# Kernel optimization log

Hardware: AMD Instinct MI355X
Metric: run time of the kernel (lower is better)

## Reference

```python
import jax, jax.numpy as jnp
import numpy as np

B, S, H = 2, 2048, 2048
E, K, HID = 8, 2, 4096          # num_experts, top-k, expert hidden (2*H)
NH, HD = 8, 256                  # attention heads, head_dim
MS, MD = 256, 512                # memory_size, memory_dim
RSTEPS, RD = 3, 512              # reasoning steps, reasoning_dim
SCALE = 16.0                     # sqrt(head_dim)


def setup_inputs() -> dict:
    key = jax.random.key(0)
    ks = iter(jax.random.split(key, 64))
    def w(shape, s=0.02):
        return (jax.random.normal(next(ks), shape, jnp.float32) * s)
    z = lambda *shape: jnp.zeros(shape, jnp.float32)
    inp = {
        'hidden_states': jax.random.normal(next(ks), (B, S, H), jnp.float32),
        'attention_mask': jnp.zeros((B, S), jnp.float32),  # 0 = unmasked (faithful: mask*-1e9 added)
        # MoE
        'gate_w': w((H, E)), 'gate_b': z(E),
        'moe_w1': w((E, H, HID)), 'moe_b1': z(E, HID),
        'moe_w2': w((E, HID, H)), 'moe_b2': z(E, H),
        # memory-augmented attention
        'q_w': w((H, H)), 'q_b': z(H),
        'k_w': w((H, H)), 'k_b': z(H),
        'v_w': w((H, H)), 'v_b': z(H),
        'o_w': w((H, H)), 'o_b': z(H),
        'mem_values': jax.random.normal(next(ks), (MS, MD), jnp.float32),
        'mem_proj_w': w((MD, H)), 'mem_proj_b': z(H),
        'mem_attn_w': w((H, MS)), 'mem_attn_b': z(MS),
        # hierarchical reasoning (stacked over steps)
        'rs_w1': w((RSTEPS, H, RD)), 'rs_b1': z(RSTEPS, RD),
        'rs_w2': w((RSTEPS, RD, H)), 'rs_b2': z(RSTEPS, H),
        'ln_g': jnp.ones((RSTEPS, H), jnp.float32), 'ln_b': z(RSTEPS, H),
        'hg_w1': w((RSTEPS, H, H // 4)), 'hg_b1': z(RSTEPS, H // 4),
        'hg_w2': w((RSTEPS, H // 4, 1)), 'hg_b2': z(RSTEPS, 1),
        'integ_w': w((RSTEPS * H, H)), 'integ_b': z(H),
    }
    return inp


def _layernorm(x, g, b, eps=1e-5):
    m = x.mean(-1, keepdims=True)
    v = ((x - m) ** 2).mean(-1, keepdims=True)
    return (x - m) / jnp.sqrt(v + eps) * g + b


def _forward(hidden_states, attention_mask, gate_w, gate_b, moe_w1, moe_b1, moe_w2, moe_b2,
             q_w, q_b, k_w, k_b, v_w, v_b, o_w, o_b, mem_values, mem_proj_w, mem_proj_b,
             mem_attn_w, mem_attn_b, rs_w1, rs_b1, rs_w2, rs_b2, ln_g, ln_b,
             hg_w1, hg_b1, hg_w2, hg_b2, integ_w, integ_b):
    h = hidden_states
    N = B * S
    # ---- Mixture of Experts (top-k routing, dense combine-weight formulation) ----
    x_flat = h.reshape(N, H)
    gate_probs = jax.nn.softmax(x_flat @ gate_w + gate_b, axis=-1)        # [N,E]
    topk_s, topk_i = jax.lax.top_k(gate_probs, K)                          # [N,K]
    topk_p = jax.nn.softmax(topk_s, axis=-1)                               # renormalize over top-k
    comb = jnp.zeros((N, E), x_flat.dtype).at[jnp.arange(N)[:, None], topk_i].add(topk_p)
    h1 = jax.nn.relu(jnp.einsum('nd,edh->neh', x_flat, moe_w1) + moe_b1)   # [N,E,HID]
    eo = jnp.einsum('neh,ehd->ned', h1, moe_w2) + moe_b2                   # [N,E,H]
    moe_out = jnp.einsum('ned,ne->nd', eo, comb).reshape(B, S, H)
    h = h + 0.5 * moe_out
    # ---- Memory-augmented attention ----
    q = (h @ q_w + q_b).reshape(B, S, NH, HD).transpose(0, 2, 1, 3)
    k = (h @ k_w + k_b).reshape(B, S, NH, HD).transpose(0, 2, 1, 3)
    v = (h @ v_w + v_b).reshape(B, S, NH, HD).transpose(0, 2, 1, 3)
    scores = jnp.einsum('bhqd,bhkd->bhqk', q, k) / SCALE
    scores = scores + attention_mask[:, None, None, :] * (-1e9)
    probs = jax.nn.softmax(scores, axis=-1)
    attn = jnp.einsum('bhqk,bhkd->bhqd', probs, v).transpose(0, 2, 1, 3).reshape(B, S, H)
    mem_p = jax.nn.softmax(h @ mem_attn_w + mem_attn_b, axis=-1)           # [B,S,MS]
    mem_o = (mem_p @ mem_values) @ mem_proj_w + mem_proj_b                 # [B,S,H]
    mem_out = (attn + 0.3 * mem_o) @ o_w + o_b
    h = h + mem_out
    # ---- Hierarchical reasoning ----
    cur = h
    outs = []
    for i in range(RSTEPS):
        so = jax.nn.relu(cur @ rs_w1[i] + rs_b1[i]) @ rs_w2[i] + rs_b2[i]
        so = _layernorm(so, ln_g[i], ln_b[i])
        g = jax.nn.sigmoid(jax.nn.relu(cur @ hg_w1[i] + hg_b1[i]) @ hg_w2[i] + hg_b2[i])  # [B,S,1]
        cur = cur + g * so
        outs.append(cur)
    final = jnp.concatenate(outs, axis=-1) @ integ_w + integ_b
    return h + final


def reference(hidden_states, attention_mask, gate_w, gate_b, moe_w1, moe_b1, moe_w2, moe_b2,
              q_w, q_b, k_w, k_b, v_w, v_b, o_w, o_b, mem_values, mem_proj_w, mem_proj_b,
              mem_attn_w, mem_attn_b, rs_w1, rs_b1, rs_w2, rs_b2, ln_g, ln_b,
              hg_w1, hg_b1, hg_w2, hg_b2, integ_w, integ_b):
    return _forward(hidden_states, attention_mask, gate_w, gate_b, moe_w1, moe_b1, moe_w2, moe_b2,
                    q_w, q_b, k_w, k_b, v_w, v_b, o_w, o_b, mem_values, mem_proj_w, mem_proj_b,
                    mem_attn_w, mem_attn_b, rs_w1, rs_b1, rs_w2, rs_b2, ln_g, ln_b,
                    hg_w1, hg_b1, hg_w2, hg_b2, integ_w, integ_b)
```

## Files before the change

### kernel.cpp

```cpp
#include <hip/hip_runtime.h>
#include <string.h>


typedef __attribute__((ext_vector_type(4))) float f32x4;
typedef __attribute__((ext_vector_type(8))) __bf16 bf16x8;

#define NTOK 4096
#define HDIM 2048
#define AS1 __attribute__((address_space(1)))
#define AS3 __attribute__((address_space(3)))

__device__ __forceinline__ unsigned short f2bf(float f) {
  unsigned u = __float_as_uint(f);
  unsigned r = (u + 0x7fffu + ((u >> 16) & 1u)) >> 16;
  return (unsigned short)r;
}
__device__ __forceinline__ float bf2f(unsigned short u) {
  return __uint_as_float(((unsigned)u) << 16);
}
__device__ __forceinline__ void unpack8(uint4 r, float* v) {
  v[0]=bf2f((unsigned short)(r.x&0xffff)); v[1]=bf2f((unsigned short)(r.x>>16));
  v[2]=bf2f((unsigned short)(r.y&0xffff)); v[3]=bf2f((unsigned short)(r.y>>16));
  v[4]=bf2f((unsigned short)(r.z&0xffff)); v[5]=bf2f((unsigned short)(r.z>>16));
  v[6]=bf2f((unsigned short)(r.w&0xffff)); v[7]=bf2f((unsigned short)(r.w>>16));
}
__device__ __forceinline__ uint4 pack8(const float* v) {
  uint4 r;
  r.x = (unsigned)f2bf(v[0]) | ((unsigned)f2bf(v[1])<<16);
  r.y = (unsigned)f2bf(v[2]) | ((unsigned)f2bf(v[3])<<16);
  r.z = (unsigned)f2bf(v[4]) | ((unsigned)f2bf(v[5])<<16);
  r.w = (unsigned)f2bf(v[6]) | ((unsigned)f2bf(v[7])<<16);
  return r;
}

__global__ void k_tconv(const float* __restrict__ in, unsigned short* __restrict__ out,
                        int R, int C, long inB, long outB) {
  __shared__ float tl[32][33];
  const int z = blockIdx.z;
  const float* ip = in + (long)z * inB;
  unsigned short* op = out + (long)z * outB;
  const int tx = threadIdx.x & 31, ty = threadIdx.x >> 5;
  const int c0 = blockIdx.x * 32, r0 = blockIdx.y * 32;
#pragma unroll
  for (int i = 0; i < 4; i++)
    tl[ty + i*8][tx] = ip[(long)(r0 + ty + i*8) * C + c0 + tx];
  __syncthreads();
#pragma unroll
  for (int i = 0; i < 4; i++)
    op[(long)(c0 + ty + i*8) * R + r0 + tx] = f2bf(tl[tx][ty + i*8]);
}

__global__ void k_tconv4(const float* __restrict__ i0, const float* __restrict__ i1,
                         const float* __restrict__ i2, const float* __restrict__ i3,
                         unsigned short* __restrict__ out) {
  __shared__ float tl[32][33];
  const int z = blockIdx.z;
  const float* ip = (z == 0) ? i0 : (z == 1) ? i1 : (z == 2) ? i2 : i3;
  unsigned short* op = out + (size_t)z * 2048 * 2048;
  const int tx = threadIdx.x & 31, ty = threadIdx.x >> 5;
  const int c0 = blockIdx.x * 32, r0 = blockIdx.y * 32;
#pragma unroll
  for (int i = 0; i < 4; i++)
    tl[ty + i*8][tx] = ip[(long)(r0 + ty + i*8) * 2048 + c0 + tx];
  __syncthreads();
#pragma unroll
  for (int i = 0; i < 4; i++)
    op[(long)(c0 + ty + i*8) * 2048 + r0 + tx] = f2bf(tl[tx][ty + i*8]);
}

__global__ void k_cvt(const float* __restrict__ in, unsigned short* __restrict__ out, long n4) {
  long i = (long)blockIdx.x * blockDim.x + threadIdx.x;
  if (i < n4) {
    float4 v = ((const float4*)in)[i];
    float vv[4] = {v.x, v.y, v.z, v.w};
    union { unsigned short u[4]; uint2 d; } p;
#pragma unroll
    for (int j = 0; j < 4; j++) p.u[j] = f2bf(vv[j]);
    ((uint2*)out)[i] = p.d;
  }
}

__global__ void k_tvact(const unsigned short* __restrict__ qkv, unsigned short* __restrict__ vT) {
  __shared__ unsigned short tl[32][33];
  const int z = blockIdx.z, b = z >> 3, hh = z & 7;
  const unsigned short* ip = qkv + (long)b * 2048 * 6144 + 4096 + hh * 256;
  unsigned short* op = vT + (long)z * 256 * 2048;
  const int tx = threadIdx.x & 31, ty = threadIdx.x >> 5;
  const int d0 = blockIdx.x * 32, s0 = blockIdx.y * 32;
#pragma unroll
  for (int i = 0; i < 4; i++)
    tl[ty + i*8][tx] = ip[(long)(s0 + ty + i*8) * 6144 + d0 + tx];
  __syncthreads();
#pragma unroll
  for (int i = 0; i < 4; i++)
    op[(long)(d0 + ty + i*8) * 2048 + s0 + tx] = tl[tx][ty + i*8];
}

__global__ void k_misc(const float* __restrict__ mask, float* __restrict__ mv,
                       const float* __restrict__ qb, const float* __restrict__ kb,
                       const float* __restrict__ vb, float* __restrict__ qkvb,
                       const float* __restrict__ rsb1, const float* __restrict__ hgb1,
                       float* __restrict__ rhb, int* __restrict__ meta) {
  const int b = blockIdx.x, t = threadIdx.x;
  if (b < 16) {
    int i = b * 256 + t; mv[i] = -1e9f * mask[i];
  } else if (b < 40) {
    int i = (b - 16) * 256 + t;
    qkvb[i] = (i < 2048) ? qb[i] : (i < 4096) ? kb[i - 2048] : vb[i - 4096];
  } else if (b < 46) {
    int i = (b - 40) * 256 + t;
    int s = i >> 9, c = i & 511;
    rhb[s * 1024 + c] = rsb1[i]; rhb[s * 1024 + 512 + c] = hgb1[i];
  } else {
    if (t < 8) meta[t] = 0;
  }
}

__global__ void k_gate(const float* __restrict__ x, const float* __restrict__ gw,
                       const float* __restrict__ gb, int* __restrict__ meta,
                       int* __restrict__ e0a, int* __restrict__ e1a,
                       float* __restrict__ w0a, float* __restrict__ w1a) {
  const int wv = threadIdx.x >> 6, ln = threadIdx.x & 63;
  const int n = blockIdx.x * 4 + wv;
  const float* xr = x + (long)n * HDIM;
  float s[8] = {0,0,0,0,0,0,0,0};
  for (int k = ln; k < HDIM; k += 64) {
    float xv = xr[k];
    const float* g = gw + (long)k * 8;
#pragma unroll
    for (int e = 0; e < 8; e++) s[e] += xv * g[e];
  }
#pragma unroll
  for (int e = 0; e < 8; e++)
    for (int d = 32; d; d >>= 1) s[e] += __shfl_xor(s[e], d);
  if (ln == 0) {
    float mx = -1e30f;
#pragma unroll
    for (int e = 0; e < 8; e++) { s[e] += gb[e]; mx = fmaxf(mx, s[e]); }
    float p[8], sum = 0.f;
#pragma unroll
    for (int e = 0; e < 8; e++) { p[e] = expf(s[e] - mx); sum += p[e]; }
    float inv = 1.f / sum;
#pragma unroll
    for (int e = 0; e < 8; e++) p[e] *= inv;
    int e0 = 0;
    for (int e = 1; e < 8; e++) if (p[e] > p[e0]) e0 = e;
    int e1 = (e0 == 0) ? 1 : 0;
    for (int e = 0; e < 8; e++) if (e != e0 && p[e] > p[e1]) e1 = e;
    float q = expf(p[e1] - p[e0]);
    float w0 = 1.f / (1.f + q), w1 = q / (1.f + q);
    e0a[n] = e0; e1a[n] = e1; w0a[n] = w0; w1a[n] = w1;
    atomicAdd(&meta[e0], 1); atomicAdd(&meta[e1], 1);
  }
}

__global__ void k_buildmap(int* meta) {
  if (threadIdx.x == 0 && blockIdx.x == 0) {
    int cum = 0, nT = 0;
    for (int e = 0; e < 8; e++) {
      int c = meta[e];
      meta[16 + e] = cum; meta[24 + e] = cum + c; meta[8 + e] = 0;
      int t = (c + 127) >> 7;
      for (int i = 0; i < t; i++) { meta[33 + nT] = e; meta[129 + nT] = cum + i * 128; nT++; }
      cum += c;
    }
    meta[32] = nT;
  }
}

__global__ void k_scatter(int* __restrict__ meta, const int* __restrict__ e0a,
                          const int* __restrict__ e1a, int* __restrict__ s0a,
                          int* __restrict__ s1a, int* __restrict__ srcTok) {
  const int n = blockIdx.x * 256 + threadIdx.x;
  if (n < NTOK) {
    int e0 = e0a[n], e1 = e1a[n];
    int s0 = meta[16 + e0] + atomicAdd(&meta[8 + e0], 1);
    int s1 = meta[16 + e1] + atomicAdd(&meta[8 + e1], 1);
    s0a[n] = s0; s1a[n] = s1; srcTok[s0] = n; srcTok[s1] = n;
  }
}

__global__ void k_combine(const float* __restrict__ h, const unsigned short* __restrict__ eo,
                          const int* __restrict__ s0a, const int* __restrict__ s1a,
                          const float* __restrict__ w0a, const float* __restrict__ w1a,
                          unsigned short* __restrict__ h2b) {
  const int n = blockIdx.x, c = threadIdx.x * 8;
  const float w0 = w0a[n], w1 = w1a[n];
  uint4 a = *(const uint4*)(eo + (long)s0a[n] * HDIM + c);
  uint4 b = *(const uint4*)(eo + (long)s1a[n] * HDIM + c);
  float va[8], vb[8]; unpack8(a, va); unpack8(b, vb);
  const float* hr = h + (long)n * HDIM + c;
  float o[8];
#pragma unroll
  for (int j = 0; j < 8; j++) o[j] = hr[j] + 0.5f * (w0 * va[j] + w1 * vb[j]);
  *(uint4*)(h2b + (long)n * HDIM + c) = pack8(o);
}

__global__ void k_softmax256(const float* __restrict__ in, unsigned short* __restrict__ out) {
  const int wv = threadIdx.x >> 6, ln = threadIdx.x & 63;
  const long r = (long)blockIdx.x * 4 + wv;
  const float4 v4 = ((const float4*)(in + r * 256))[ln];
  float v[4] = {v4.x, v4.y, v4.z, v4.w};
  float m = fmaxf(fmaxf(v[0], v[1]), fmaxf(v[2], v[3]));
  for (int d = 32; d; d >>= 1) m = fmaxf(m, __shfl_xor(m, d));
  float s = 0.f;
#pragma unroll
  for (int j = 0; j < 4; j++) { v[j] = expf(v[j] - m); s += v[j]; }
  for (int d = 32; d; d >>= 1) s += __shfl_xor(s, d);
  const float inv = 1.f / s;
  union { unsigned short u[4]; uint2 d2; } p;
#pragma unroll
  for (int j = 0; j < 4; j++) p.u[j] = f2bf(v[j] * inv);
  ((uint2*)(out + r * 256))[ln] = p.d2;
}

__global__ void k_gdot(const unsigned short* __restrict__ g1, long ld, const float* __restrict__ w,
                       const float* __restrict__ bb, float* __restrict__ gv) {
  const int wv = threadIdx.x >> 6, ln = threadIdx.x & 63;
  const int n = blockIdx.x * 4 + wv;
  uint4 raw = *(const uint4*)(g1 + (long)n * ld + ln * 8);
  float v[8]; unpack8(raw, v);
  const float4 wa = ((const float4*)w)[ln * 2];
  const float4 wb = ((const float4*)w)[ln * 2 + 1];
  float s = v[0]*wa.x + v[1]*wa.y + v[2]*wa.z + v[3]*wa.w
          + v[4]*wb.x + v[5]*wb.y + v[6]*wb.z + v[7]*wb.w;
  for (int d = 32; d; d >>= 1) s += __shfl_xor(s, d);
  if (ln == 0) gv[n] = 1.f / (1.f + expf(-(s + bb[0])));
}

__global__ void k_lnupdate(const float* __restrict__ so, const float* __restrict__ curIn,
                           const float* __restrict__ gv, const float* __restrict__ lng,
                           const float* __restrict__ lnb, float* __restrict__ curOut,
                           unsigned short* __restrict__ curbOut, unsigned short* __restrict__ outs,
                           int step) {
  const int n = blockIdx.x, t = threadIdx.x, wv = t >> 6, ln = t & 63, c = t * 8;
  const float* row = so + (long)n * 2048 + c;
  float x[8];
#pragma unroll
  for (int j = 0; j < 8; j++) x[j] = row[j];
  float s1 = 0.f, s2 = 0.f;
#pragma unroll
  for (int j = 0; j < 8; j++) { s1 += x[j]; s2 += x[j] * x[j]; }
  for (int d = 32; d; d >>= 1) { s1 += __shfl_xor(s1, d); s2 += __shfl_xor(s2, d); }
  __shared__ float a1[4], a2[4];
  if (ln == 0) { a1[wv] = s1; a2[wv] = s2; }
  __syncthreads();
  s1 = a1[0] + a1[1] + a1[2] + a1[3];
  s2 = a2[0] + a2[1] + a2[2] + a2[3];
  const float mean = s1 * (1.f / 2048.f);
  const float var = s2 * (1.f / 2048.f) - mean * mean;
  const float rstd = rsqrtf(var + 1e-5f);
  const float g = gv[n];
  const float* ci = curIn + (long)n * 2048 + c;
  float o[8];
#pragma unroll
  for (int j = 0; j < 8; j++) {
    float l = (x[j] - mean) * rstd * lng[c + j] + lnb[c + j];
    o[j] = ci[j] + g * l;
  }
  float* co = curOut + (long)n * 2048 + c;
#pragma unroll
  for (int j = 0; j < 8; j++) co[j] = o[j];
  *(uint4*)(curbOut + (long)n * 2048 + c) = pack8(o);
  *(uint4*)(outs + (long)n * 6144 + (long)step * 2048 + c) = pack8(o);
}

struct GArgs {
  const unsigned short* A; long lda, aSO, aSI;
  const unsigned short* Bt; long ldb, bSO, bSI;
  int M, N, K;
  const float* adv; long advSO, advSI;
  float alpha, rscale;
  const float* rF; long ldrF, rfSO, rfSI;
  const unsigned short* rB; long ldrB, rbSO, rbSI;
  float* oF; long ldoF, ofSO, ofSI;
  unsigned short* oB; long ldoB, obSO, obSI;
  const int* meta;
  const int* srcTok;
};

template <int MOE, int RELU, int RESID, int OUTF, int OUTB>
__global__ __launch_bounds__(512) void gemm_bt(GArgs g) {
  __shared__ unsigned short lds[2 * 16384];
  const int t = threadIdx.x, wv = t >> 6, ln = t & 63, ln15 = ln & 15;
  const int lr8 = ln >> 3;
  const int lsl = (ln & 7) ^ lr8;
  const int bz = blockIdx.z;
  int row0, rowMax;
  const unsigned short *A, *Bt;
  long advO = 0, rFO = 0, rBO = 0, oFO = 0, oBO = 0;
  if constexpr (MOE) {
    const int ty = blockIdx.y;
    if (ty >= g.meta[32]) return;
    const int e = g.meta[33 + ty];
    row0 = g.meta[129 + ty]; rowMax = g.meta[24 + e];
    A = g.A; Bt = g.Bt + (long)e * g.bSO;
    advO = (long)e * g.advSO;
  } else {
    row0 = blockIdx.y << 7; rowMax = g.M;
    const long bo = (long)(bz >> 3), bi = (long)(bz & 7);
    A = g.A + bo * g.aSO + bi * g.aSI;
    Bt = g.Bt + bo * g.bSO + bi * g.bSI;
    advO = bo * g.advSO + bi * g.advSI;
    rFO = bo * g.rfSO + bi * g.rfSI;
    rBO = bo * g.rbSO + bi * g.rbSI;
    oFO = bo * g.ofSO + bi * g.ofSI;
    oBO = bo * g.obSO + bi * g.obSI;
  }
  const int col0 = blockIdx.x << 7;
  const long lda = g.lda, ldb = g.ldb;
  const int wm = (wv >> 2) << 6;
  const int wc = (wv & 3) << 5;

  int grow0, grow1;
  {
    int r0i = row0 + (wv << 4) + lr8;
    int r1i = r0i + 8;
    if constexpr (MOE) {
      r0i = (r0i < rowMax) ? r0i : (rowMax - 1);
      r1i = (r1i < rowMax) ? r1i : (rowMax - 1);
    }
    if constexpr (MOE == 2) { grow0 = g.srcTok[r0i]; grow1 = g.srcTok[r1i]; }
    else { grow0 = r0i; grow1 = r1i; }
  }

  auto STAGE = [&](int kt, unsigned base) {
    const long kk = ((long)kt << 6) + (lsl << 3);
    {
      const int rb = (wv << 4);
      __builtin_amdgcn_global_load_lds(
          (const AS1 void*)(A + (long)grow0 * lda + kk),
          (AS3 void*)(lds + base + (rb << 6)), 16, 0, 0);
      __builtin_amdgcn_global_load_lds(
          (const AS1 void*)(A + (long)grow1 * lda + kk),
          (AS3 void*)(lds + base + ((rb + 8) << 6)), 16, 0, 0);
    }
#pragma unroll
    for (int l = 0; l < 2; ++l) {
      const int rb = (wv << 4) + (l << 3);
      __builtin_amdgcn_global_load_lds(
          (const AS1 void*)(Bt + (long)(col0 + rb + lr8) * ldb + kk),
          (AS3 void*)(lds + base + 8192 + (rb << 6)), 16, 0, 0);
    }
  };

  const f32x4 fz = {0.f, 0.f, 0.f, 0.f};
  f32x4 acc[4][2];
#pragma unroll
  for (int i = 0; i < 4; i++)
#pragma unroll
    for (int j = 0; j < 2; j++) acc[i][j] = fz;

  const int nt = g.K >> 6;

  STAGE(0, 0);
  asm volatile("s_waitcnt vmcnt(0)" ::: "memory");
  __builtin_amdgcn_s_barrier();

  for (int kt = 0; kt < nt; ++kt) {
    const unsigned aB = (kt & 1) ? 16384u : 0u;
    const unsigned nB = aB ^ 16384u;
    if (kt + 1 < nt) STAGE(kt + 1, nB);
#pragma unroll
    for (int ks = 0; ks < 2; ++ks) {
      const int kb = (ks << 2) + (ln >> 4);
      bf16x8 bg[2];
#pragma unroll
      for (int j = 0; j < 2; ++j) {
        const int r = wc + (j << 4) + ln15;
        bg[j] = *(const bf16x8*)(lds + aB + 8192 + (r << 6) + ((kb ^ (r & 7)) << 3));
      }
      __builtin_amdgcn_s_setprio(1);
#pragma unroll
      for (int i = 0; i < 4; ++i) {
        const int r = wm + (i << 4) + ln15;
        bf16x8 a = *(const bf16x8*)(lds + aB + (r << 6) + ((kb ^ (r & 7)) << 3));
#pragma unroll
        for (int j = 0; j < 2; ++j)
          acc[i][j] = __builtin_amdgcn_mfma_f32_16x16x32_bf16(a, bg[j], acc[i][j], 0, 0, 0);
      }
      __builtin_amdgcn_s_setprio(0);
    }
    asm volatile("s_waitcnt vmcnt(0)" ::: "memory");
    __builtin_amdgcn_s_barrier();
  }

#pragma unroll
  for (int i = 0; i < 4; i++) {
#pragma unroll
    for (int j = 0; j < 2; j++) {
      const int cc = col0 + wc + (j << 4) + ln15;
      const float av = g.adv ? g.adv[advO + cc] : 0.f;
#pragma unroll
      for (int r = 0; r < 4; r++) {
        const int rr = row0 + wm + (i << 4) + ((ln >> 4) << 2) + r;
        if (rr < rowMax) {
          float v = g.alpha * acc[i][j][r] + av;
          if constexpr (RELU) v = fmaxf(v, 0.f);
          if constexpr (RESID == 1) v = g.rF[rFO + (long)rr * g.ldrF + cc] + g.rscale * v;
          if constexpr (RESID == 2) v = bf2f(g.rB[rBO + (long)rr * g.ldrB + cc]) + g.rscale * v;
          if constexpr (OUTF) g.oF[oFO + (long)rr * g.ldoF + cc] = v;
          if constexpr (OUTB) g.oB[oBO + (long)rr * g.ldoB + cc] = f2bf(v);
        }
      }
    }
  }
}

__global__ __launch_bounds__(512) void k_pv(const unsigned short* __restrict__ S,
                                            const unsigned short* __restrict__ Vt,
                                            unsigned short* __restrict__ O) {
  __shared__ unsigned short lds[4096 + 16384];
  __shared__ float pm[64][8], ps[64][8];
  __shared__ float smax[64], sinv[64];
  const int t = threadIdx.x, wv = t >> 6, ln = t & 63, ln15 = ln & 15;
  const int lr8 = ln >> 3, lk = ln & 7;
  const int lsl = lk ^ lr8;
  const int rt = blockIdx.x, bh = blockIdx.y;
  const int b = bh >> 3, hh = bh & 7;
  const int row0 = rt << 6;
  const unsigned short* Sb = S + (long)bh * 2048 * 2048;
  const unsigned short* Vb = Vt + (long)bh * 256 * 2048;

  {
    const int r = t >> 3, sg = t & 7;
    const unsigned short* p = Sb + (long)(row0 + r) * 2048 + sg * 256;
    float m = -3.0e38f, s = 0.f;
    for (int i = 0; i < 32; ++i) {
      uint4 raw = ((const uint4*)p)[i];
      float v[8]; unpack8(raw, v);
      float m8 = v[0];
#pragma unroll
      for (int j = 1; j < 8; j++) m8 = fmaxf(m8, v[j]);
      const float mn = fmaxf(m, m8);
      s *= expf(m - mn);
#pragma unroll
      for (int j = 0; j < 8; j++) s += expf(v[j] - mn);
      m = mn;
    }
    pm[r][sg] = m; ps[r][sg] = s;
  }
  __syncthreads();
  if (t < 64) {
    float m = pm[t][0];
#pragma unroll
    for (int j = 1; j < 8; j++) m = fmaxf(m, pm[t][j]);
    float s = 0.f;
#pragma unroll
    for (int j = 0; j < 8; j++) s += ps[t][j] * expf(pm[t][j] - m);
    smax[t] = m; sinv[t] = 1.f / s;
  }
  __syncthreads();
  const int arow = (wv << 3) + lr8;
  const float am = smax[arow], ainv = sinv[arow];

  const f32x4 fz = {0.f, 0.f, 0.f, 0.f};
  f32x4 acc[4][2];
#pragma unroll
  for (int i = 0; i < 4; i++)
#pragma unroll
    for (int j = 0; j < 2; j++) acc[i][j] = fz;

  const int wc = wv << 5;

  for (int kt = 0; kt < 32; ++kt) {
    const long kk = ((long)kt << 6) + (lsl << 3);
    const uint4 araw = *(const uint4*)(Sb + (long)(row0 + arow) * 2048 + kk);
#pragma unroll
    for (int l = 0; l < 4; ++l) {
      const int rb = (l << 6) + (wv << 3);
      __builtin_amdgcn_global_load_lds(
          (const AS1 void*)(Vb + (long)(rb + lr8) * 2048 + kk),
          (AS3 void*)(lds + 4096 + (rb << 6)), 16, 0, 0);
    }
    {
      float v[8]; unpack8(araw, v);
      float pvv[8];
#pragma unroll
      for (int j = 0; j < 8; j++) pvv[j] = expf(v[j] - am) * ainv;
      *(uint4*)(lds + (arow << 6) + (lk << 3)) = pack8(pvv);
    }
    __syncthreads();
#pragma unroll
    for (int ks = 0; ks < 2; ++ks) {
      const int kb = (ks << 2) + (ln >> 4);
      bf16x8 bg[2];
#pragma unroll
      for (int j = 0; j < 2; ++j) {
        const int r = wc + (j << 4) + ln15;
        bg[j] = *(const bf16x8*)(lds + 4096 + (r << 6) + ((kb ^ (r & 7)) << 3));
      }
      __builtin_amdgcn_s_setprio(1);
#pragma unroll
      for (int i = 0; i < 4; ++i) {
        const int r = (i << 4) + ln15;
        bf16x8 a = *(const bf16x8*)(lds + (r << 6) + ((kb ^ (r & 7)) << 3));
#pragma unroll
        for (int j = 0; j < 2; ++j)
          acc[i][j] = __builtin_amdgcn_mfma_f32_16x16x32_bf16(a, bg[j], acc[i][j], 0, 0, 0);
      }
      __builtin_amdgcn_s_setprio(0);
    }
    __syncthreads();
  }

  unsigned short* Ob = O + (long)b * 2048 * 2048 + hh * 256;
#pragma unroll
  for (int i = 0; i < 4; ++i) {
#pragma unroll
    for (int j = 0; j < 2; ++j) {
      const int cc = wc + (j << 4) + ln15;
#pragma unroll
      for (int r = 0; r < 4; ++r) {
        const int rr = row0 + (i << 4) + ((ln >> 4) << 2) + r;
        Ob[(long)rr * 2048 + cc] = f2bf(acc[i][j][r]);
      }
    }
  }
}

static constexpr size_t O_W1T = 0;
static constexpr size_t O_W2T = O_W1T + (size_t)8 * 4096 * 2048 * 2;
static constexpr size_t O_QT  = O_W2T + (size_t)8 * 4096 * 2048 * 2;
static constexpr size_t O_KT  = O_QT + (size_t)2048 * 2048 * 2;
static constexpr size_t O_VWT = O_KT + (size_t)2048 * 2048 * 2;
static constexpr size_t O_OT  = O_VWT + (size_t)2048 * 2048 * 2;
static constexpr size_t O_MAT = O_OT + (size_t)2048 * 2048 * 2;
static constexpr size_t O_MPT = O_MAT + (size_t)256 * 2048 * 2;
static constexpr size_t O_MVT = O_MPT + (size_t)2048 * 512 * 2;
static constexpr size_t O_RH1 = O_MVT + (size_t)512 * 256 * 2;
static constexpr size_t O_RS2 = O_RH1 + (size_t)3 * 1024 * 2048 * 2;
static constexpr size_t O_IGT = O_RS2 + (size_t)3 * 2048 * 512 * 2;
static constexpr size_t O_META= O_IGT + (size_t)2048 * 6144 * 2;
static constexpr size_t O_E0  = O_META + 4096;
static constexpr size_t O_E1  = O_E0 + 16384;
static constexpr size_t O_W0  = O_E1 + 16384;
static constexpr size_t O_W1  = O_W0 + 16384;
static constexpr size_t O_S0  = O_W1 + 16384;
static constexpr size_t O_S1  = O_S0 + 16384;
static constexpr size_t O_SRC = O_S1 + 16384;
static constexpr size_t O_MSK = O_SRC + 32768;
static constexpr size_t O_GV  = O_MSK + 16384;
static constexpr size_t O_QKVB= O_GV + 16384;
static constexpr size_t O_RHB = O_QKVB + 6144 * 4;
static constexpr size_t O_H2  = O_RHB + 3072 * 4;
static constexpr size_t O_H2B = O_H2 + (size_t)4096 * 2048 * 4;
static constexpr size_t O_H3  = O_H2B + (size_t)4096 * 2048 * 2;
static constexpr size_t O_H3B = O_H3 + (size_t)4096 * 2048 * 4;
static constexpr size_t O_ATT = O_H3B + (size_t)4096 * 2048 * 2;
static constexpr size_t O_AO2 = O_ATT + (size_t)4096 * 2048 * 2;
static constexpr size_t O_MLG = O_AO2 + (size_t)4096 * 2048 * 2;
static constexpr size_t O_MPB = O_MLG + (size_t)4096 * 256 * 4;
static constexpr size_t O_MPV = O_MPB + (size_t)4096 * 256 * 2;
static constexpr size_t O_AR  = O_MPV + (size_t)4096 * 512 * 2;
static constexpr size_t O_XB = O_AR;
static constexpr size_t O_XG = O_XB + (size_t)4096 * 2048 * 2;
static constexpr size_t O_H1 = O_XG + (size_t)8192 * 2048 * 2;
static constexpr size_t O_EO = O_H1 + (size_t)8192 * 4096 * 2;
static constexpr size_t O_QB = O_AR;
static constexpr size_t O_VT = O_QB + (size_t)3 * 4096 * 2048 * 2;
static constexpr size_t O_SC = O_VT + (size_t)4096 * 2048 * 2;
static constexpr size_t O_T1 = O_AR;
static constexpr size_t O_SOB= O_T1 + (size_t)4096 * 1024 * 2;
static constexpr size_t O_CUR= O_SOB + (size_t)4096 * 2048 * 4;
static constexpr size_t O_CRB= O_CUR + (size_t)4096 * 2048 * 4;
static constexpr size_t O_OUS= O_CRB + (size_t)4096 * 2048 * 2;

extern "C" void kernel_launch(void* const* d_in, const int* in_sizes, int n_in,
                              void* d_out, int out_size, void* d_ws, size_t ws_size,
                              hipStream_t stream) {
  (void)in_sizes; (void)n_in; (void)out_size; (void)ws_size;
  const float* h        = (const float*)d_in[0];
  const float* mask     = (const float*)d_in[1];
  const float* gate_w   = (const float*)d_in[2];
  const float* gate_b   = (const float*)d_in[3];
  const float* moe_w1   = (const float*)d_in[4];
  const float* moe_b1   = (const float*)d_in[5];
  const float* moe_w2   = (const float*)d_in[6];
  const float* moe_b2   = (const float*)d_in[7];
  const float* q_w      = (const float*)d_in[8];
  const float* q_b      = (const float*)d_in[9];
  const float* k_w      = (const float*)d_in[10];
  const float* k_b      = (const float*)d_in[11];
  const float* v_w      = (const float*)d_in[12];
  const float* v_b      = (const float*)d_in[13];
  const float* o_w      = (const float*)d_in[14];
  const float* o_b      = (const float*)d_in[15];
  const float* mem_vals = (const float*)d_in[16];
  const float* mproj_w  = (const float*)d_in[17];
  const float* mproj_b  = (const float*)d_in[18];
  const float* mattn_w  = (const float*)d_in[19];
  const float* mattn_b  = (const float*)d_in[20];
  const float* rs_w1    = (const float*)d_in[21];
  const float* rs_b1    = (const float*)d_in[22];
  const float* rs_w2    = (const float*)d_in[23];
  const float* rs_b2    = (const float*)d_in[24];
  const float* ln_g     = (const float*)d_in[25];
  const float* ln_b     = (const float*)d_in[26];
  const float* hg_w1    = (const float*)d_in[27];
  const float* hg_b1    = (const float*)d_in[28];
  const float* hg_w2    = (const float*)d_in[29];
  const float* hg_b2    = (const float*)d_in[30];
  const float* integ_w  = (const float*)d_in[31];
  const float* integ_b  = (const float*)d_in[32];

  char* ws = (char*)d_ws;
  auto U = [&](size_t o) { return (unsigned short*)(ws + o); };
  auto F = [&](size_t o) { return (float*)(ws + o); };
  auto I = [&](size_t o) { return (int*)(ws + o); };

  k_tconv<<<dim3(128, 64, 8), 256, 0, stream>>>(moe_w1, U(O_W1T), 2048, 4096, 8388608, 8388608);
  k_tconv<<<dim3(64, 128, 8), 256, 0, stream>>>(moe_w2, U(O_W2T), 4096, 2048, 8388608, 8388608);
  k_tconv4<<<dim3(64, 64, 4), 256, 0, stream>>>(q_w, k_w, v_w, o_w, U(O_QT));
  k_tconv<<<dim3(8, 64, 1), 256, 0, stream>>>(mattn_w, U(O_MAT), 2048, 256, 0, 0);
  k_tconv<<<dim3(64, 16, 1), 256, 0, stream>>>(mproj_w, U(O_MPT), 512, 2048, 0, 0);
  k_tconv<<<dim3(16, 8, 1), 256, 0, stream>>>(mem_vals, U(O_MVT), 256, 512, 0, 0);
  k_tconv<<<dim3(16, 64, 3), 256, 0, stream>>>(rs_w1, U(O_RH1), 2048, 512, 2048 * 512, 1024 * 2048);
  k_tconv<<<dim3(16, 64, 3), 256, 0, stream>>>(hg_w1, U(O_RH1) + (size_t)512 * 2048, 2048, 512,
                                               2048 * 512, 1024 * 2048);
  k_tconv<<<dim3(64, 16, 3), 256, 0, stream>>>(rs_w2, U(O_RS2), 512, 2048, 512 * 2048, 512 * 2048);
  k_tconv<<<dim3(64, 192, 1), 256, 0, stream>>>(integ_w, U(O_IGT), 6144, 2048, 0, 0);
  k_cvt<<<8192, 256, 0, stream>>>(h, U(O_XB), 2097152);
  k_misc<<<47, 256, 0, stream>>>(mask, F(O_MSK), q_b, k_b, v_b, F(O_QKVB),
                                 rs_b1, hg_b1, F(O_RHB), I(O_META));

  k_gate<<<1024, 256, 0, stream>>>(h, gate_w, gate_b, I(O_META), I(O_E0), I(O_E1), F(O_W0), F(O_W1));
  k_buildmap<<<1, 1, 0, stream>>>(I(O_META));
  k_scatter<<<16, 256, 0, stream>>>(I(O_META), I(O_E0), I(O_E1), I(O_S0), I(O_S1), I(O_SRC));

  GArgs z0; memset(&z0, 0, sizeof(z0)); z0.alpha = 1.f; z0.rscale = 1.f;
  {
    GArgs g = z0;
    g.A = U(O_XB); g.lda = 2048;
    g.Bt = U(O_W1T); g.ldb = 2048; g.bSO = (long)4096 * 2048;
    g.N = 4096; g.K = 2048;
    g.adv = moe_b1; g.advSO = 4096;
    g.oB = U(O_H1); g.ldoB = 4096;
    g.meta = I(O_META); g.srcTok = I(O_SRC);
    gemm_bt<2, 1, 0, 0, 1><<<dim3(32, 72, 1), 512, 0, stream>>>(g);
  }
  {
    GArgs g = z0;
    g.A = U(O_H1); g.lda = 4096;
    g.Bt = U(O_W2T); g.ldb = 4096; g.bSO = (long)2048 * 4096;
    g.N = 2048; g.K = 4096;
    g.adv = moe_b2; g.advSO = 2048;
    g.oB = U(O_EO); g.ldoB = 2048;
    g.meta = I(O_META);
    gemm_bt<1, 0, 0, 0, 1><<<dim3(16, 72, 1), 512, 0, stream>>>(g);
  }
  k_combine<<<4096, 256, 0, stream>>>(h, U(O_EO), I(O_S0), I(O_S1), F(O_W0), F(O_W1), U(O_H2B));

  {
    GArgs g = z0;
    g.A = U(O_H2B); g.lda = 2048; g.M = 4096; g.N = 6144; g.K = 2048;
    g.Bt = U(O_QT); g.ldb = 2048;
    g.adv = F(O_QKVB);
    g.oB = U(O_QB); g.ldoB = 6144;
    gemm_bt<0, 0, 0, 0, 1><<<dim3(48, 32, 1), 512, 0, stream>>>(g);
  }
  k_tvact<<<dim3(8, 64, 16), 256, 0, stream>>>(U(O_QB), U(O_VT));
  {
    GArgs g = z0;
    g.A = U(O_QB); g.lda = 6144; g.aSO = 12582912; g.aSI = 256;
    g.Bt = U(O_QB) + 2048; g.ldb = 6144; g.bSO = 12582912; g.bSI = 256;
    g.M = 2048; g.N = 2048; g.K = 256;
    g.adv = F(O_MSK); g.advSO = 2048; g.advSI = 0;
    g.alpha = 0.0625f;
    g.oB = U(O_SC); g.ldoB = 2048; g.obSO = 33554432; g.obSI = 4194304;
    gemm_bt<0, 0, 0, 0, 1><<<dim3(16, 16, 16), 512, 0, stream>>>(g);
  }
  k_pv<<<dim3(32, 16, 1), 512, 0, stream>>>(U(O_SC), U(O_VT), U(O_ATT));
  {
    GArgs g = z0;
    g.A = U(O_H2B); g.lda = 2048; g.Bt = U(O_MAT); g.ldb = 2048;
    g.M = 4096; g.N = 256; g.K = 2048;
    g.adv = mattn_b;
    g.oF = F(O_MLG); g.ldoF = 256;
    gemm_bt<0, 0, 0, 1, 0><<<dim3(2, 32, 1), 512, 0, stream>>>(g);
  }
  k_softmax256<<<1024, 256, 0, stream>>>(F(O_MLG), U(O_MPB));
  {
    GArgs g = z0;
    g.A = U(O_MPB); g.lda = 256; g.Bt = U(O_MVT); g.ldb = 256;
    g.M = 4096; g.N = 512; g.K = 256;
    g.oB = U(O_MPV); g.ldoB = 512;
    gemm_bt<0, 0, 0, 0, 1><<<dim3(4, 32, 1), 512, 0, stream>>>(g);
  }
  {
    GArgs g = z0;
    g.A = U(O_MPV); g.lda = 512; g.Bt = U(O_MPT); g.ldb = 512;
    g.M = 4096; g.N = 2048; g.K = 512;
    g.adv = mproj_b;
    g.rB = U(O_ATT); g.ldrB = 2048; g.rscale = 0.3f;
    g.oB = U(O_AO2); g.ldoB = 2048;
    gemm_bt<0, 0, 2, 0, 1><<<dim3(16, 32, 1), 512, 0, stream>>>(g);
  }
  {
    GArgs g = z0;
    g.A = U(O_AO2); g.lda = 2048; g.Bt = U(O_OT); g.ldb = 2048;
    g.M = 4096; g.N = 2048; g.K = 2048;
    g.adv = o_b;
    g.rB = U(O_H2B); g.ldrB = 2048; g.rscale = 1.f;
    g.oF = F(O_H3); g.ldoF = 2048;
    g.oB = U(O_H3B); g.ldoB = 2048;
    gemm_bt<0, 0, 2, 1, 1><<<dim3(16, 32, 1), 512, 0, stream>>>(g);
  }

  for (int i = 0; i < 3; i++) {
    const unsigned short* curb = (i == 0) ? U(O_H3B) : U(O_CRB);
    const float* curf = (i == 0) ? F(O_H3) : F(O_CUR);
    {
      GArgs g = z0;
      g.A = curb; g.lda = 2048;
      g.Bt = U(O_RH1) + (size_t)i * 1024 * 2048; g.ldb = 2048;
      g.M = 4096; g.N = 1024; g.K = 2048;
      g.adv = F(O_RHB) + i * 1024;
      g.oB = U(O_T1); g.ldoB = 1024;
      gemm_bt<0, 1, 0, 0, 1><<<dim3(8, 32, 1), 512, 0, stream>>>(g);
    }
    {
      GArgs g = z0;
      g.A = U(O_T1); g.lda = 1024;
      g.Bt = U(O_RS2) + (size_t)i * 2048 * 512; g.ldb = 512;
      g.M = 4096; g.N = 2048; g.K = 512;
      g.adv = rs_b2 + i * 2048;
      g.oF = F(O_SOB); g.ldoF = 2048;
      gemm_bt<0, 0, 0, 1, 0><<<dim3(16, 32, 1), 512, 0, stream>>>(g);
    }
    k_gdot<<<1024, 256, 0, stream>>>(U(O_T1) + 512, 1024, hg_w2 + i * 512, hg_b2 + i, F(O_GV));
    k_lnupdate<<<4096, 256, 0, stream>>>(F(O_SOB), curf, F(O_GV), ln_g + i * 2048,
                                         ln_b + i * 2048, F(O_CUR), U(O_CRB), U(O_OUS), i);
  }
  {
    GArgs g = z0;
    g.A = U(O_OUS); g.lda = 6144; g.Bt = U(O_IGT); g.ldb = 6144;
    g.M = 4096; g.N = 2048; g.K = 6144;
    g.adv = integ_b;
    g.rF = F(O_H3); g.ldrF = 2048; g.rscale = 1.f;
    g.oF = (float*)d_out; g.ldoF = 2048;
    gemm_bt<0, 0, 1, 1, 0><<<dim3(16, 32, 1), 512, 0, stream>>>(g);
  }
}
```

Measured before the change: 1.677 ms.

## Use 4-wave 64x64 warp tiles with BK=32 in shared bf16 GEMM

The generic GEMM moves from 8 waves (512 threads) with 64x32 per-wave tiles and a K-step of 64 to 4 waves (256 threads) with 64x64 per-wave tiles and a K-step of 32. The smaller LDS footprint (32 KB double-buffered) and launch_bounds(256,4) aim for more resident blocks per CU. Larger per-wave tiles raise MFMA-to-LDS-read reuse. The cost is twice as many K iterations, each with its own barrier, and more accumulator registers per lane; the LDS swizzle is reworked to match the 64-byte row stride.

Measured after the change: 1.890 ms. 12.7% more time.

```diff
diff --git a/kernel.cpp b/kernel.cpp
--- a/kernel.cpp
+++ b/kernel.cpp
@@ -280,11 +280,10 @@
 };
 
 template <int MOE, int RELU, int RESID, int OUTF, int OUTB>
-__global__ __launch_bounds__(512) void gemm_bt(GArgs g) {
-  __shared__ unsigned short lds[2 * 16384];
+__global__ __launch_bounds__(256, 4) void gemm_bt(GArgs g) {
+  __shared__ unsigned short lds[2 * 8192];
   const int t = threadIdx.x, wv = t >> 6, ln = t & 63, ln15 = ln & 15;
-  const int lr8 = ln >> 3;
-  const int lsl = (ln & 7) ^ lr8;
+  const int lsl = (ln & 3) ^ ((ln >> 3) & 3);
   const int bz = blockIdx.z;
   int row0, rowMax;
   const unsigned short *A, *Bt;
@@ -309,74 +308,70 @@
   }
   const int col0 = blockIdx.x << 7;
   const long lda = g.lda, ldb = g.ldb;
-  const int wm = (wv >> 2) << 6;
-  const int wc = (wv & 3) << 5;
-
-  int grow0, grow1;
-  {
-    int r0i = row0 + (wv << 4) + lr8;
-    int r1i = r0i + 8;
+  const int wm = (wv >> 1) << 6, wc = (wv & 1) << 6;
+
+  int grow0, grow1, brow0, brow1;
+  {
+    int r0i = row0 + (wv << 5) + (ln >> 2);
+    int r1i = r0i + 16;
     if constexpr (MOE) {
       r0i = (r0i < rowMax) ? r0i : (rowMax - 1);
       r1i = (r1i < rowMax) ? r1i : (rowMax - 1);
     }
     if constexpr (MOE == 2) { grow0 = g.srcTok[r0i]; grow1 = g.srcTok[r1i]; }
     else { grow0 = r0i; grow1 = r1i; }
+    brow0 = col0 + (wv << 5) + (ln >> 2);
+    brow1 = brow0 + 16;
   }
 
   auto STAGE = [&](int kt, unsigned base) {
-    const long kk = ((long)kt << 6) + (lsl << 3);
-    {
-      const int rb = (wv << 4);
-      __builtin_amdgcn_global_load_lds(
-          (const AS1 void*)(A + (long)grow0 * lda + kk),
-          (AS3 void*)(lds + base + (rb << 6)), 16, 0, 0);
-      __builtin_amdgcn_global_load_lds(
-          (const AS1 void*)(A + (long)grow1 * lda + kk),
-          (AS3 void*)(lds + base + ((rb + 8) << 6)), 16, 0, 0);
-    }
-#pragma unroll
-    for (int l = 0; l < 2; ++l) {
-      const int rb = (wv << 4) + (l << 3);
-      __builtin_amdgcn_global_load_lds(
-          (const AS1 void*)(Bt + (long)(col0 + rb + lr8) * ldb + kk),
-          (AS3 void*)(lds + base + 8192 + (rb << 6)), 16, 0, 0);
-    }
+    const long kk = ((long)kt << 5) + (lsl << 3);
+    __builtin_amdgcn_global_load_lds(
+        (const AS1 void*)(A + (long)grow0 * lda + kk),
+        (AS3 void*)(lds + base + ((wv << 5) << 5)), 16, 0, 0);
+    __builtin_amdgcn_global_load_lds(
+        (const AS1 void*)(A + (long)grow1 * lda + kk),
+        (AS3 void*)(lds + base + (((wv << 5) + 16) << 5)), 16, 0, 0);
+    __builtin_amdgcn_global_load_lds(
+        (const AS1 void*)(Bt + (long)brow0 * ldb + kk),
+        (AS3 void*)(lds + base + 4096 + ((wv << 5) << 5)), 16, 0, 0);
+    __builtin_amdgcn_global_load_lds(
+        (const AS1 void*)(Bt + (long)brow1 * ldb + kk),
+        (AS3 void*)(lds + base + 4096 + (((wv << 5) + 16) << 5)), 16, 0, 0);
   };
 
   const f32x4 fz = {0.f, 0.f, 0.f, 0.f};
-  f32x4 acc[4][2];
+  f32x4 acc[4][4];
 #pragma unroll
   for (int i = 0; i < 4; i++)
 #pragma unroll
-    for (int j = 0; j < 2; j++) acc[i][j] = fz;
-
-  const int nt = g.K >> 6;
+    for (int j = 0; j < 4; j++) acc[i][j] = fz;
+
+  const int nt = g.K >> 5;
+  const int kb = ln >> 4;
 
   STAGE(0, 0);
   asm volatile("s_waitcnt vmcnt(0)" ::: "memory");
   __builtin_amdgcn_s_barrier();
 
   for (int kt = 0; kt < nt; ++kt) {
-    const unsigned aB = (kt & 1) ? 16384u : 0u;
-    const unsigned nB = aB ^ 16384u;
+    const unsigned aB = (kt & 1) ? 8192u : 0u;
+    const unsigned nB = aB ^ 8192u;
     if (kt + 1 < nt) STAGE(kt + 1, nB);
-#pragma unroll
-    for (int ks = 0; ks < 2; ++ks) {
-      const int kb = (ks << 2) + (ln >> 4);
-      bf16x8 bg[2];
-#pragma unroll
-      for (int j = 0; j < 2; ++j) {
+    {
+      bf16x8 bg[4];
+#pragma unroll
+      for (int j = 0; j < 4; ++j) {
         const int r = wc + (j << 4) + ln15;
-        bg[j] = *(const bf16x8*)(lds + aB + 8192 + (r << 6) + ((kb ^ (r & 7)) << 3));
+        bg[j] = *(const bf16x8*)(lds + aB + 4096 + (r << 5) + ((kb ^ ((r >> 1) & 3)) << 3));
       }
       __builtin_amdgcn_s_setprio(1);
 #pragma unroll
       for (int i = 0; i < 4; ++i) {
         const int r = wm + (i << 4) + ln15;
-        bf16x8 a = *(const bf16x8*)(lds + aB + (r << 6) + ((kb ^ (r & 7)) << 3));
-#pragma unroll
-        for (int j = 0; j < 2; ++j)
+        bf16x8 a = *(const bf16x8*)(lds + aB + (r << 5) + ((kb ^ ((r >> 1) & 3)) << 3));
+#pragma unroll
+        for (int j = 0; j < 4; ++j)
           acc[i][j] = __builtin_amdgcn_mfma_f32_16x16x32_bf16(a, bg[j], acc[i][j], 0, 0, 0);
       }
       __builtin_amdgcn_s_setprio(0);
@@ -388,7 +383,7 @@
 #pragma unroll
   for (int i = 0; i < 4; i++) {
 #pragma unroll
-    for (int j = 0; j < 2; j++) {
+    for (int j = 0; j < 4; j++) {
       const int cc = col0 + wc + (j << 4) + ln15;
       const float av = g.adv ? g.adv[advO + cc] : 0.f;
 #pragma unroll
@@ -637,7 +632,7 @@
     g.adv = moe_b1; g.advSO = 4096;
     g.oB = U(O_H1); g.ldoB = 4096;
     g.meta = I(O_META); g.srcTok = I(O_SRC);
-    gemm_bt<2, 1, 0, 0, 1><<<dim3(32, 72, 1), 512, 0, stream>>>(g);
+    gemm_bt<2, 1, 0, 0, 1><<<dim3(32, 72, 1), 256, 0, stream>>>(g);
   }
   {
     GArgs g = z0;
@@ -647,7 +642,7 @@
     g.adv = moe_b2; g.advSO = 2048;
     g.oB = U(O_EO); g.ldoB = 2048;
     g.meta = I(O_META);
-    gemm_bt<1, 0, 0, 0, 1><<<dim3(16, 72, 1), 512, 0, stream>>>(g);
+    gemm_bt<1, 0, 0, 0, 1><<<dim3(16, 72, 1), 256, 0, stream>>>(g);
   }
   k_combine<<<4096, 256, 0, stream>>>(h, U(O_EO), I(O_S0), I(O_S1), F(O_W0), F(O_W1), U(O_H2B));
 
@@ -657,7 +652,7 @@
     g.Bt = U(O_QT); g.ldb = 2048;
     g.adv = F(O_QKVB);
     g.oB = U(O_QB); g.ldoB = 6144;
-    gemm_bt<0, 0, 0, 0, 1><<<dim3(48, 32, 1), 512, 0, stream>>>(g);
+    gemm_bt<0, 0, 0, 0, 1><<<dim3(48, 32, 1), 256, 0, stream>>>(g);
   }
   k_tvact<<<dim3(8, 64, 16), 256, 0, stream>>>(U(O_QB), U(O_VT));
   {
@@ -668,7 +663,7 @@
     g.adv = F(O_MSK); g.advSO = 2048; g.advSI = 0;
     g.alpha = 0.0625f;
     g.oB = U(O_SC); g.ldoB = 2048; g.obSO = 33554432; g.obSI = 4194304;
-    gemm_bt<0, 0, 0, 0, 1><<<dim3(16, 16, 16), 512, 0, stream>>>(g);
+    gemm_bt<0, 0, 0, 0, 1><<<dim3(16, 16, 16), 256, 0, stream>>>(g);
   }
   k_pv<<<dim3(32, 16, 1), 512, 0, stream>>>(U(O_SC), U(O_VT), U(O_ATT));
   {
@@ -677,7 +672,7 @@
     g.M = 4096; g.N = 256; g.K = 2048;
     g.adv = mattn_b;
     g.oF = F(O_MLG); g.ldoF = 256;
-    gemm_bt<0, 0, 0, 1, 0><<<dim3(2, 32, 1), 512, 0, stream>>>(g);
+    gemm_bt<0, 0, 0, 1, 0><<<dim3(2, 32, 1), 256, 0, stream>>>(g);
   }
   k_softmax256<<<1024, 256, 0, stream>>>(F(O_MLG), U(O_MPB));
   {
@@ -685,7 +680,7 @@
     g.A = U(O_MPB); g.lda = 256; g.Bt = U(O_MVT); g.ldb = 256;
     g.M = 4096; g.N = 512; g.K = 256;
     g.oB = U(O_MPV); g.ldoB = 512;
-    gemm_bt<0, 0, 0, 0, 1><<<dim3(4, 32, 1), 512, 0, stream>>>(g);
+    gemm_bt<0, 0, 0, 0, 1><<<dim3(4, 32, 1), 256, 0, stream>>>(g);
   }
   {
     GArgs g = z0;
@@ -694,7 +689,7 @@
     g.adv = mproj_b;
     g.rB = U(O_ATT); g.ldrB = 2048; g.rscale = 0.3f;
     g.oB = U(O_AO2); g.ldoB = 2048;
-    gemm_bt<0, 0, 2, 0, 1><<<dim3(16, 32, 1), 512, 0, stream>>>(g);
+    gemm_bt<0, 0, 2, 0, 1><<<dim3(16, 32, 1), 256, 0, stream>>>(g);
   }
   {
     GArgs g = z0;
@@ -704,7 +699,7 @@
     g.rB = U(O_H2B); g.ldrB = 2048; g.rscale = 1.f;
     g.oF = F(O_H3); g.ldoF = 2048;
     g.oB = U(O_H3B); g.ldoB = 2048;
-    gemm_bt<0, 0, 2, 1, 1><<<dim3(16, 32, 1), 512, 0, stream>>>(g);
+    gemm_bt<0, 0, 2, 1, 1><<<dim3(16, 32, 1), 256, 0, stream>>>(g);
   }
 
   for (int i = 0; i < 3; i++) {
@@ -717,7 +712,7 @@
       g.M = 4096; g.N = 1024; g.K = 2048;
       g.adv = F(O_RHB) + i * 1024;
       g.oB = U(O_T1); g.ldoB = 1024;
-      gemm_bt<0, 1, 0, 0, 1><<<dim3(8, 32, 1), 512, 0, stream>>>(g);
+      gemm_bt<0, 1, 0, 0, 1><<<dim3(8, 32, 1), 256, 0, stream>>>(g);
     }
     {
       GArgs g = z0;
@@ -726,7 +721,7 @@
       g.M = 4096; g.N = 2048; g.K = 512;
       g.adv = rs_b2 + i * 2048;
       g.oF = F(O_SOB); g.ldoF = 2048;
-      gemm_bt<0, 0, 0, 1, 0><<<dim3(16, 32, 1), 512, 0, stream>>>(g);
+      gemm_bt<0, 0, 0, 1, 0><<<dim3(16, 32, 1), 256, 0, stream>>>(g);
     }
     k_gdot<<<1024, 256, 0, stream>>>(U(O_T1) + 512, 1024, hg_w2 + i * 512, hg_b2 + i, F(O_GV));
     k_lnupdate<<<4096, 256, 0, stream>>>(F(O_SOB), curf, F(O_GV), ln_g + i * 2048,
@@ -739,6 +734,6 @@
     g.adv = integ_b;
     g.rF = F(O_H3); g.ldrF = 2048; g.rscale = 1.f;
     g.oF = (float*)d_out; g.ldoF = 2048;
-    gemm_bt<0, 0, 1, 1, 0><<<dim3(16, 32, 1), 512, 0, stream>>>(g);
-  }
-}
+    gemm_bt<0, 0, 1, 1, 0><<<dim3(16, 32, 1), 256, 0, stream>>>(g);
+  }
+}
```

## Fuse bf16 input conversion into gate and keep residual stream in bf16

Applied to the files above, without the earlier changes.

Removes the standalone fp32-to-bf16 conversion kernel by writing the bf16 copy of the input inside the gating kernel. Drops the fp32 copies of the residual stream (H3, cur) and stores the reasoning step output in bf16, so the layernorm-update kernel reads and writes only bf16. The final integration GEMM now takes its residual from bf16. This cuts memory traffic and one launch, at the cost of lower precision in the residual path and the layernorm inputs. The workspace layout is also compacted.

New measurement: 1.592 ms. -5.1%, faster.

```diff
diff --git a/kernel.cpp b/kernel.cpp
--- a/kernel.cpp
+++ b/kernel.cpp
@@ -66,18 +66,6 @@
 #pragma unroll
   for (int i = 0; i < 4; i++)
     op[(long)(c0 + ty + i*8) * 2048 + r0 + tx] = f2bf(tl[tx][ty + i*8]);
-}
-
-__global__ void k_cvt(const float* __restrict__ in, unsigned short* __restrict__ out, long n4) {
-  long i = (long)blockIdx.x * blockDim.x + threadIdx.x;
-  if (i < n4) {
-    float4 v = ((const float4*)in)[i];
-    float vv[4] = {v.x, v.y, v.z, v.w};
-    union { unsigned short u[4]; uint2 d; } p;
-#pragma unroll
-    for (int j = 0; j < 4; j++) p.u[j] = f2bf(vv[j]);
-    ((uint2*)out)[i] = p.d;
-  }
 }
 
 __global__ void k_tvact(const unsigned short* __restrict__ qkv, unsigned short* __restrict__ vT) {
@@ -119,13 +107,16 @@
 __global__ void k_gate(const float* __restrict__ x, const float* __restrict__ gw,
                        const float* __restrict__ gb, int* __restrict__ meta,
                        int* __restrict__ e0a, int* __restrict__ e1a,
-                       float* __restrict__ w0a, float* __restrict__ w1a) {
+                       float* __restrict__ w0a, float* __restrict__ w1a,
+                       unsigned short* __restrict__ xb) {
   const int wv = threadIdx.x >> 6, ln = threadIdx.x & 63;
   const int n = blockIdx.x * 4 + wv;
   const float* xr = x + (long)n * HDIM;
+  unsigned short* xo = xb + (long)n * HDIM;
   float s[8] = {0,0,0,0,0,0,0,0};
   for (int k = ln; k < HDIM; k += 64) {
     float xv = xr[k];
+    xo[k] = f2bf(xv);
     const float* g = gw + (long)k * 8;
 #pragma unroll
     for (int e = 0; e < 8; e++) s[e] += xv * g[e];
@@ -228,16 +219,15 @@
   if (ln == 0) gv[n] = 1.f / (1.f + expf(-(s + bb[0])));
 }
 
-__global__ void k_lnupdate(const float* __restrict__ so, const float* __restrict__ curIn,
+__global__ void k_lnupdate(const unsigned short* __restrict__ so,
+                           const unsigned short* __restrict__ curIn,
                            const float* __restrict__ gv, const float* __restrict__ lng,
-                           const float* __restrict__ lnb, float* __restrict__ curOut,
-                           unsigned short* __restrict__ curbOut, unsigned short* __restrict__ outs,
-                           int step) {
+                           const float* __restrict__ lnb,
+                           unsigned short* __restrict__ curbOut,
+                           unsigned short* __restrict__ outs, int step) {
   const int n = blockIdx.x, t = threadIdx.x, wv = t >> 6, ln = t & 63, c = t * 8;
-  const float* row = so + (long)n * 2048 + c;
-  float x[8];
-#pragma unroll
-  for (int j = 0; j < 8; j++) x[j] = row[j];
+  uint4 raw = *(const uint4*)(so + (long)n * 2048 + c);
+  float x[8]; unpack8(raw, x);
   float s1 = 0.f, s2 = 0.f;
 #pragma unroll
   for (int j = 0; j < 8; j++) { s1 += x[j]; s2 += x[j] * x[j]; }
@@ -251,18 +241,17 @@
   const float var = s2 * (1.f / 2048.f) - mean * mean;
   const float rstd = rsqrtf(var + 1e-5f);
   const float g = gv[n];
-  const float* ci = curIn + (long)n * 2048 + c;
+  uint4 ci = *(const uint4*)(curIn + (long)n * 2048 + c);
+  float cv[8]; unpack8(ci, cv);
   float o[8];
 #pragma unroll
   for (int j = 0; j < 8; j++) {
     float l = (x[j] - mean) * rstd * lng[c + j] + lnb[c + j];
-    o[j] = ci[j] + g * l;
-  }
-  float* co = curOut + (long)n * 2048 + c;
-#pragma unroll
-  for (int j = 0; j < 8; j++) co[j] = o[j];
-  *(uint4*)(curbOut + (long)n * 2048 + c) = pack8(o);
-  *(uint4*)(outs + (long)n * 6144 + (long)step * 2048 + c) = pack8(o);
+    o[j] = cv[j] + g * l;
+  }
+  const uint4 pk = pack8(o);
+  *(uint4*)(curbOut + (long)n * 2048 + c) = pk;
+  *(uint4*)(outs + (long)n * 6144 + (long)step * 2048 + c) = pk;
 }
 
 struct GArgs {
@@ -522,10 +511,7 @@
 static constexpr size_t O_W1T = 0;
 static constexpr size_t O_W2T = O_W1T + (size_t)8 * 4096 * 2048 * 2;
 static constexpr size_t O_QT  = O_W2T + (size_t)8 * 4096 * 2048 * 2;
-static constexpr size_t O_KT  = O_QT + (size_t)2048 * 2048 * 2;
-static constexpr size_t O_VWT = O_KT + (size_t)2048 * 2048 * 2;
-static constexpr size_t O_OT  = O_VWT + (size_t)2048 * 2048 * 2;
-static constexpr size_t O_MAT = O_OT + (size_t)2048 * 2048 * 2;
+static constexpr size_t O_MAT = O_QT + (size_t)4 * 2048 * 2048 * 2;
 static constexpr size_t O_MPT = O_MAT + (size_t)256 * 2048 * 2;
 static constexpr size_t O_MVT = O_MPT + (size_t)2048 * 512 * 2;
 static constexpr size_t O_RH1 = O_MVT + (size_t)512 * 256 * 2;
@@ -543,10 +529,8 @@
 static constexpr size_t O_GV  = O_MSK + 16384;
 static constexpr size_t O_QKVB= O_GV + 16384;
 static constexpr size_t O_RHB = O_QKVB + 6144 * 4;
-static constexpr size_t O_H2  = O_RHB + 3072 * 4;
-static constexpr size_t O_H2B = O_H2 + (size_t)4096 * 2048 * 4;
-static constexpr size_t O_H3  = O_H2B + (size_t)4096 * 2048 * 2;
-static constexpr size_t O_H3B = O_H3 + (size_t)4096 * 2048 * 4;
+static constexpr size_t O_H2B = O_RHB + 3072 * 4;
+static constexpr size_t O_H3B = O_H2B + (size_t)4096 * 2048 * 2;
 static constexpr size_t O_ATT = O_H3B + (size_t)4096 * 2048 * 2;
 static constexpr size_t O_AO2 = O_ATT + (size_t)4096 * 2048 * 2;
 static constexpr size_t O_MLG = O_AO2 + (size_t)4096 * 2048 * 2;
@@ -554,16 +538,14 @@
 static constexpr size_t O_MPV = O_MPB + (size_t)4096 * 256 * 2;
 static constexpr size_t O_AR  = O_MPV + (size_t)4096 * 512 * 2;
 static constexpr size_t O_XB = O_AR;
-static constexpr size_t O_XG = O_XB + (size_t)4096 * 2048 * 2;
-static constexpr size_t O_H1 = O_XG + (size_t)8192 * 2048 * 2;
+static constexpr size_t O_H1 = O_XB + (size_t)4096 * 2048 * 2 + (size_t)8192 * 2048 * 2;
 static constexpr size_t O_EO = O_H1 + (size_t)8192 * 4096 * 2;
-static constexpr size_t O_QB = O_AR;
+static constexpr size_t O_QB = O_XB + (size_t)4096 * 2048 * 2;
 static constexpr size_t O_VT = O_QB + (size_t)3 * 4096 * 2048 * 2;
 static constexpr size_t O_SC = O_VT + (size_t)4096 * 2048 * 2;
-static constexpr size_t O_T1 = O_AR;
+static constexpr size_t O_T1 = O_QB;
 static constexpr size_t O_SOB= O_T1 + (size_t)4096 * 1024 * 2;
-static constexpr size_t O_CUR= O_SOB + (size_t)4096 * 2048 * 4;
-static constexpr size_t O_CRB= O_CUR + (size_t)4096 * 2048 * 4;
+static constexpr size_t O_CRB= O_SOB + (size_t)4096 * 2048 * 2;
 static constexpr size_t O_OUS= O_CRB + (size_t)4096 * 2048 * 2;
 
 extern "C" void kernel_launch(void* const* d_in, const int* in_sizes, int n_in,
@@ -620,11 +602,11 @@
                                                2048 * 512, 1024 * 2048);
   k_tconv<<<dim3(64, 16, 3), 256, 0, stream>>>(rs_w2, U(O_RS2), 512, 2048, 512 * 2048, 512 * 2048);
   k_tconv<<<dim3(64, 192, 1), 256, 0, stream>>>(integ_w, U(O_IGT), 6144, 2048, 0, 0);
-  k_cvt<<<8192, 256, 0, stream>>>(h, U(O_XB), 2097152);
   k_misc<<<47, 256, 0, stream>>>(mask, F(O_MSK), q_b, k_b, v_b, F(O_QKVB),
                                  rs_b1, hg_b1, F(O_RHB), I(O_META));
 
-  k_gate<<<1024, 256, 0, stream>>>(h, gate_w, gate_b, I(O_META), I(O_E0), I(O_E1), F(O_W0), F(O_W1));
+  k_gate<<<1024, 256, 0, stream>>>(h, gate_w, gate_b, I(O_META), I(O_E0), I(O_E1),
+                                   F(O_W0), F(O_W1), U(O_XB));
   k_buildmap<<<1, 1, 0, stream>>>(I(O_META));
   k_scatter<<<16, 256, 0, stream>>>(I(O_META), I(O_E0), I(O_E1), I(O_S0), I(O_S1), I(O_SRC));
 
@@ -698,18 +680,16 @@
   }
   {
     GArgs g = z0;
-    g.A = U(O_AO2); g.lda = 2048; g.Bt = U(O_OT); g.ldb = 2048;
+    g.A = U(O_AO2); g.lda = 2048; g.Bt = U(O_QT) + (size_t)3 * 2048 * 2048; g.ldb = 2048;
     g.M = 4096; g.N = 2048; g.K = 2048;
     g.adv = o_b;
     g.rB = U(O_H2B); g.ldrB = 2048; g.rscale = 1.f;
-    g.oF = F(O_H3); g.ldoF = 2048;
     g.oB = U(O_H3B); g.ldoB = 2048;
-    gemm_bt<0, 0, 2, 1, 1><<<dim3(16, 32, 1), 512, 0, stream>>>(g);
+    gemm_bt<0, 0, 2, 0, 1><<<dim3(16, 32, 1), 512, 0, stream>>>(g);
   }
 
   for (int i = 0; i < 3; i++) {
     const unsigned short* curb = (i == 0) ? U(O_H3B) : U(O_CRB);
-    const float* curf = (i == 0) ? F(O_H3) : F(O_CUR);
     {
       GArgs g = z0;
       g.A = curb; g.lda = 2048;
@@ -725,20 +705,20 @@
       g.Bt = U(O_RS2) + (size_t)i * 2048 * 512; g.ldb = 512;
       g.M = 4096; g.N = 2048; g.K = 512;
       g.adv = rs_b2 + i * 2048;
-      g.oF = F(O_SOB); g.ldoF = 2048;
-      gemm_bt<0, 0, 0, 1, 0><<<dim3(16, 32, 1), 512, 0, stream>>>(g);
+      g.oB = U(O_SOB); g.ldoB = 2048;
+      gemm_bt<0, 0, 0, 0, 1><<<dim3(16, 32, 1), 512, 0, stream>>>(g);
     }
     k_gdot<<<1024, 256, 0, stream>>>(U(O_T1) + 512, 1024, hg_w2 + i * 512, hg_b2 + i, F(O_GV));
-    k_lnupdate<<<4096, 256, 0, stream>>>(F(O_SOB), curf, F(O_GV), ln_g + i * 2048,
-                                         ln_b + i * 2048, F(O_CUR), U(O_CRB), U(O_OUS), i);
+    k_lnupdate<<<4096, 256, 0, stream>>>(U(O_SOB), curb, F(O_GV), ln_g + i * 2048,
+                                         ln_b + i * 2048, U(O_CRB), U(O_OUS), i);
   }
   {
     GArgs g = z0;
     g.A = U(O_OUS); g.lda = 6144; g.Bt = U(O_IGT); g.ldb = 6144;
     g.M = 4096; g.N = 2048; g.K = 6144;
     g.adv = integ_b;
-    g.rF = F(O_H3); g.ldrF = 2048; g.rscale = 1.f;
+    g.rB = U(O_H3B); g.ldrB = 2048; g.rscale = 1.f;
     g.oF = (float*)d_out; g.ldoF = 2048;
-    gemm_bt<0, 0, 1, 1, 0><<<dim3(16, 32, 1), 512, 0, stream>>>(g);
-  }
-}
+    gemm_bt<0, 0, 2, 1, 0><<<dim3(16, 32, 1), 512, 0, stream>>>(g);
+  }
+}
```
